# Performance work log

Hardware: AMD Instinct MI355X
Metric: run time of the kernel (lower is better)

## Reference

```python
import jax, jax.numpy as jnp
import numpy as np

EMBED = 384   # embeddingSize
BLOCK = 256   # blockSize (max T, also actual T here)
HEAD = 64     # headSize
B = 512
NEG_INF = -1e9  # stands in for float('-inf'); safe under fp16/bf16 via finite large value


def setup_inputs() -> dict:
    key = jax.random.key(0)
    k1, k2, k3, k4 = jax.random.split(key, 4)
    input = jax.random.normal(k1, (B, BLOCK, EMBED), dtype=jnp.float32)
    # nn.Linear(EMBED, HEAD, bias=False) weights, stored transposed for x @ W
    s = 1.0 / np.sqrt(EMBED)
    Wk = jax.random.uniform(k2, (EMBED, HEAD), dtype=jnp.float32, minval=-s, maxval=s)
    Wq = jax.random.uniform(k3, (EMBED, HEAD), dtype=jnp.float32, minval=-s, maxval=s)
    Wv = jax.random.uniform(k4, (EMBED, HEAD), dtype=jnp.float32, minval=-s, maxval=s)
    return {"input": input, "Wk": Wk, "Wq": Wq, "Wv": Wv}


def reference(input, Wk, Wq, Wv):
    B_, T, C = input.shape
    k = input @ Wk  # (B, T, H)
    q = input @ Wq  # (B, T, H)
    v = input @ Wv  # (B, T, H)
    # NOTE: original scales by C**-0.5 where C = embedding size (384), not head size.
    scale = jnp.asarray(C, input.dtype) ** -0.5
    weight = jnp.einsum('bth,bsh->bts', q, k) * scale  # (B, Tq, Tk)
    causal = jnp.tril(jnp.ones((T, T), dtype=bool))    # tril[:T,:T]
    weight = jnp.where(causal, weight, NEG_INF)
    # NOTE: original applies softmax over dim=1 (the QUERY axis), faithfully reproduced.
    weight = jax.nn.softmax(weight, axis=1)
    # dropout is identity in eval mode (deterministic reference)
    output = jnp.einsum('bts,bsh->bth', weight, v)     # (B, T, H)
    return output
```

## Files before the change

kernel.cpp:

```cpp
#include <hip/hip_runtime.h>
#include <hip/hip_bf16.h>

#define TT 256
#define CE 384
#define HD 64

typedef __attribute__((ext_vector_type(8))) short short8v;
typedef __attribute__((ext_vector_type(4))) float float4v;
typedef __attribute__((ext_vector_type(4))) unsigned int uint4v;
typedef __attribute__((ext_vector_type(4))) unsigned short ushort4v;

#define SCALE 0.05103103630798287f

__device__ __forceinline__ unsigned short f2bf(float f) {
    union { __hip_bfloat16 b; unsigned short u; } cv;
    cv.b = __float2bfloat16(f);
    return cv.u;
}
__device__ __forceinline__ unsigned int pk2(float a, float b) {
    return (unsigned int)f2bf(a) | ((unsigned int)f2bf(b) << 16);
}

__device__ __forceinline__ int adr8(int row, int col) {
    return row * 128 + ((((col >> 3) ^ (row & 7)) & 7) << 4) + ((col & 7) << 1);
}

#define BAR() do {                                            \
    asm volatile("s_waitcnt lgkmcnt(0)" ::: "memory");        \
    __builtin_amdgcn_s_barrier();                             \
    __builtin_amdgcn_sched_barrier(0);                        \
} while (0)

__global__ void wprep(const float* __restrict__ Wk, const float* __restrict__ Wq,
                      const float* __restrict__ Wv, unsigned short* __restrict__ Wt) {
    int idx = blockIdx.x * 256 + threadIdx.x;
    if (idx >= 3 * HD * CE) return;
    int w = idx / (HD * CE);
    int rem = idx - w * (HD * CE);
    int h = rem / CE;
    int c = rem - h * CE;
    const float* W = (w == 0) ? Wk : (w == 1) ? Wq : Wv;
    Wt[idx] = f2bf(W[c * HD + h]);
}

__global__ __launch_bounds__(512, 4)
void qkv(const float* __restrict__ X, const unsigned short* __restrict__ Wt,
         unsigned short* __restrict__ Kb, unsigned short* __restrict__ Qb,
         unsigned short* __restrict__ Vt) {
    __shared__ char lds[40960];
    char* Xs = lds;
    char* Ws = lds + 16384;

    const int bid = blockIdx.x;
    const int b = bid >> 1, rh = bid & 1;
    const int tid = threadIdx.x;
    const int w = tid >> 6, l = tid & 63;
    const int l15 = l & 15, lq = l >> 4;

    const float* Xb = X + ((long)b * TT + rh * 128) * CE;

    const int xt0 = tid >> 3,        xk0 = tid & 7;
    const int xt1 = 64 + (tid >> 3), xk1 = tid & 7;
    const int wn0 = tid >> 3;
    const int wn1 = 64 + (tid >> 3);
    const int wn2 = 128 + (tid >> 3);
    const int wk = tid & 7;

    float4 xa0, xa1, xb0, xb1;
    uint4v wr0, wr1, wr2;

    auto issue = [&](int kk) {
        const float* s0 = Xb + xt0 * CE + kk + xk0 * 8;
        xa0 = *(const float4*)s0;  xa1 = *(const float4*)(s0 + 4);
        const float* s1 = Xb + xt1 * CE + kk + xk1 * 8;
        xb0 = *(const float4*)s1;  xb1 = *(const float4*)(s1 + 4);
        wr0 = *(const uint4v*)(Wt + wn0 * CE + kk + wk * 8);
        wr1 = *(const uint4v*)(Wt + wn1 * CE + kk + wk * 8);
        wr2 = *(const uint4v*)(Wt + wn2 * CE + kk + wk * 8);
    };
    auto store = [&]() {
        uint4v p0 = {pk2(xa0.x, xa0.y), pk2(xa0.z, xa0.w), pk2(xa1.x, xa1.y), pk2(xa1.z, xa1.w)};
        *(uint4v*)(Xs + xt0 * 128 + (((xk0 ^ (xt0 & 7)) & 7) << 4)) = p0;
        uint4v p1 = {pk2(xb0.x, xb0.y), pk2(xb0.z, xb0.w), pk2(xb1.x, xb1.y), pk2(xb1.z, xb1.w)};
        *(uint4v*)(Xs + xt1 * 128 + (((xk1 ^ (xt1 & 7)) & 7) << 4)) = p1;
        *(uint4v*)(Ws + wn0 * 128 + (((wk ^ (wn0 & 7)) & 7) << 4)) = wr0;
        *(uint4v*)(Ws + wn1 * 128 + (((wk ^ (wn1 & 7)) & 7) << 4)) = wr1;
        *(uint4v*)(Ws + wn2 * 128 + (((wk ^ (wn2 & 7)) & 7) << 4)) = wr2;
    };

    const float4v fzero = {0.f, 0.f, 0.f, 0.f};
    float4v acc[12];
    #pragma unroll
    for (int j = 0; j < 12; ++j) acc[j] = fzero;

    issue(0);
    for (int kc = 0; kc < 6; ++kc) {
        BAR();
        store();
        if (kc < 5) issue((kc + 1) * 64);
        BAR();
        #pragma unroll
        for (int ks = 0; ks < 2; ++ks) {
            short8v a = *(const short8v*)(Xs + adr8(w * 16 + l15, ks * 32 + lq * 8));
            #pragma unroll
            for (int nt = 0; nt < 12; ++nt) {
                short8v bb = *(const short8v*)(Ws + adr8(nt * 16 + l15, ks * 32 + lq * 8));
                acc[nt] = __builtin_amdgcn_mfma_f32_16x16x32_bf16(a, bb, acc[nt], 0, 0, 0);
            }
        }
    }

    const int t0 = rh * 128 + w * 16 + lq * 4;
    #pragma unroll
    for (int nt = 0; nt < 12; ++nt) {
        const int n = nt * 16 + l15;
        if (n < 64) {
            #pragma unroll
            for (int r = 0; r < 4; ++r)
                Kb[((long)b * TT + t0 + r) * HD + n] = f2bf(acc[nt][r]);
        } else if (n < 128) {
            const int h = n - 64;
            #pragma unroll
            for (int r = 0; r < 4; ++r)
                Qb[((long)b * TT + t0 + r) * HD + h] = f2bf(acc[nt][r]);
        } else {
            const int h = n - 128;
            ushort4v pv;
            pv[0] = f2bf(acc[nt][0]);
            pv[1] = f2bf(acc[nt][1]);
            pv[2] = f2bf(acc[nt][2]);
            pv[3] = f2bf(acc[nt][3]);
            *(ushort4v*)(Vt + ((long)b * HD + h) * TT + t0) = pv;
        }
    }
}

__global__ __launch_bounds__(512, 4)
void attn(const unsigned short* __restrict__ Kb, const unsigned short* __restrict__ Qb,
          const unsigned short* __restrict__ Vt, float* __restrict__ out) {
    extern __shared__ char lds[];
    char* Qs  = lds;
    char* Wts = lds + 32768;
    char* Ks  = lds + 65536;
    char* Vts = lds + 73728;
    float2* smx = (float2*)Ks;

    const int b = blockIdx.x;
    const int tid = threadIdx.x;
    const int w = tid >> 6, l = tid & 63;
    const int l15 = l & 15, lq = l >> 4;
    const int sw = w & 3, th = w >> 2;

    #pragma unroll
    for (int j = 0; j < 4; ++j) {
        int ci = j * 512 + tid;
        int t = ci >> 3, k8 = ci & 7;
        uint4v p = *(const uint4v*)(Qb + ((long)b * TT + t) * HD + k8 * 8);
        *(uint4v*)(Qs + t * 128 + (((k8 ^ (t & 7)) & 7) << 4)) = p;
    }

    const float4v fzero = {0.f, 0.f, 0.f, 0.f};
    float4v o[2][4];
    #pragma unroll
    for (int i = 0; i < 2; ++i)
        #pragma unroll
        for (int j = 0; j < 4; ++j) o[i][j] = fzero;

    const int vrow = tid >> 3, vc8 = tid & 7;

    for (int sb = 0; sb < 4; ++sb) {
        const int s0 = sb * 64;
        __syncthreads();
        {
            uint4v pk = *(const uint4v*)(Kb + ((long)b * TT + s0 + vrow) * HD + vc8 * 8);
            *(uint4v*)(Ks + vrow * 128 + (((vc8 ^ (vrow & 7)) & 7) << 4)) = pk;
            uint4v pv = *(const uint4v*)(Vt + ((long)b * HD + vrow) * TT + s0 + vc8 * 8);
            *(uint4v*)(Vts + vrow * 128 + (((vc8 ^ (vrow & 7)) & 7) << 4)) = pv;
        }
        __syncthreads();

        float4v z[8];
        #pragma unroll
        for (int tt = 0; tt < 8; ++tt) z[tt] = fzero;
        #pragma unroll
        for (int ks = 0; ks < 2; ++ks) {
            short8v ak = *(const short8v*)(Ks + adr8(sw * 16 + l15, ks * 32 + lq * 8));
            #pragma unroll
            for (int tt = 0; tt < 8; ++tt) {
                short8v bq = *(const short8v*)(Qs + adr8(th * 128 + tt * 16 + l15, ks * 32 + lq * 8));
                z[tt] = __builtin_amdgcn_mfma_f32_16x16x32_bf16(ak, bq, z[tt], 0, 0, 0);
            }
        }
        __syncthreads();

        float pm[4], fac[4];
        #pragma unroll
        for (int r = 0; r < 4; ++r) {
            const int s = s0 + sw * 16 + lq * 4 + r;
            float mm = -1e30f;
            #pragma unroll
            for (int tt = 0; tt < 8; ++tt) {
                int t = th * 128 + tt * 16 + l15;
                float v = (t >= s) ? z[tt][r] * SCALE : -1e30f;
                z[tt][r] = v;
                mm = fmaxf(mm, v);
            }
            mm = fmaxf(mm, __shfl_xor(mm, 1));
            mm = fmaxf(mm, __shfl_xor(mm, 2));
            mm = fmaxf(mm, __shfl_xor(mm, 4));
            mm = fmaxf(mm, __shfl_xor(mm, 8));
            float ps = 0.f;
            #pragma unroll
            for (int tt = 0; tt < 8; ++tt) {
                float p = (z[tt][r] > -1e29f) ? __expf(z[tt][r] - mm) : 0.f;
                z[tt][r] = p;
                ps += p;
            }
            ps += __shfl_xor(ps, 1);
            ps += __shfl_xor(ps, 2);
            ps += __shfl_xor(ps, 4);
            ps += __shfl_xor(ps, 8);
            pm[r] = mm;
            if (l15 == 0) smx[th * 64 + sw * 16 + lq * 4 + r] = make_float2(mm, ps);
        }
        __syncthreads();

        #pragma unroll
        for (int r = 0; r < 4; ++r) {
            const int row = sw * 16 + lq * 4 + r;
            float2 h0 = smx[row];
            float2 h1 = smx[64 + row];
            float m = fmaxf(h0.x, h1.x);
            float denom = h0.y * __expf(h0.x - m) + h1.y * __expf(h1.x - m);
            fac[r] = __expf(pm[r] - m) / denom;
        }

        #pragma unroll
        for (int tt = 0; tt < 8; ++tt) {
            const int t = th * 128 + tt * 16 + l15;
            const int col = sw * 16 + lq * 4;
            ushort4v pw;
            pw[0] = f2bf(z[tt][0] * fac[0]);
            pw[1] = f2bf(z[tt][1] * fac[1]);
            pw[2] = f2bf(z[tt][2] * fac[2]);
            pw[3] = f2bf(z[tt][3] * fac[3]);
            *(ushort4v*)(Wts + t * 128 + ((((col >> 3) ^ (t & 7)) & 7) << 4) + ((col & 7) << 1)) = pw;
        }
        __syncthreads();

        #pragma unroll
        for (int ks = 0; ks < 2; ++ks) {
            short8v aw0 = *(const short8v*)(Wts + adr8(w * 32 + l15,      ks * 32 + lq * 8));
            short8v aw1 = *(const short8v*)(Wts + adr8(w * 32 + 16 + l15, ks * 32 + lq * 8));
            #pragma unroll
            for (int ht = 0; ht < 4; ++ht) {
                short8v bv = *(const short8v*)(Vts + adr8(ht * 16 + l15, ks * 32 + lq * 8));
                o[0][ht] = __builtin_amdgcn_mfma_f32_16x16x32_bf16(aw0, bv, o[0][ht], 0, 0, 0);
                o[1][ht] = __builtin_amdgcn_mfma_f32_16x16x32_bf16(aw1, bv, o[1][ht], 0, 0, 0);
            }
        }
    }

    #pragma unroll
    for (int rt = 0; rt < 2; ++rt)
        #pragma unroll
        for (int ht = 0; ht < 4; ++ht) {
            int t0 = w * 32 + rt * 16 + lq * 4;
            int h = ht * 16 + l15;
            #pragma unroll
            for (int r = 0; r < 4; ++r)
                out[((long)b * TT + t0 + r) * HD + h] = o[rt][ht][r];
        }
}

extern "C" void kernel_launch(void* const* d_in, const int* in_sizes, int n_in,
                              void* d_out, int out_size, void* d_ws, size_t ws_size,
                              hipStream_t stream) {
    const float* X  = (const float*)d_in[0];
    const float* Wk = (const float*)d_in[1];
    const float* Wq = (const float*)d_in[2];
    const float* Wv = (const float*)d_in[3];
    float* out = (float*)d_out;

    char* ws = (char*)d_ws;
    unsigned short* Wt = (unsigned short*)ws;
    unsigned short* Kb = (unsigned short*)(ws + 147456);
    unsigned short* Qb = (unsigned short*)(ws + 147456 + 16777216L);
    unsigned short* Vt = (unsigned short*)(ws + 147456 + 2 * 16777216L);

    (void)hipFuncSetAttribute(reinterpret_cast<const void*>(attn),
                              hipFuncAttributeMaxDynamicSharedMemorySize, 81920);

    wprep<<<288, 256, 0, stream>>>(Wk, Wq, Wv, Wt);
    qkv<<<1024, 512, 0, stream>>>(X, Wt, Kb, Qb, Vt);
    attn<<<512, 512, 81920, stream>>>(Kb, Qb, Vt, out);
}
```

Baseline: 85.55 us.

## Double-buffer LDS in qkv and prefetch K/V tiles in attn with priority hints

Result: slower. 109.0 us (+27.4%).

```diff
diff --git a/kernel.cpp b/kernel.cpp
--- a/kernel.cpp
+++ b/kernel.cpp
@@ -47,9 +47,7 @@
 void qkv(const float* __restrict__ X, const unsigned short* __restrict__ Wt,
          unsigned short* __restrict__ Kb, unsigned short* __restrict__ Qb,
          unsigned short* __restrict__ Vt) {
-    __shared__ char lds[40960];
-    char* Xs = lds;
-    char* Ws = lds + 16384;
+    extern __shared__ char lds[];
 
     const int bid = blockIdx.x;
     const int b = bid >> 1, rh = bid & 1;
@@ -66,23 +64,40 @@
     const int wn2 = 128 + (tid >> 3);
     const int wk = tid & 7;
 
-    float4 xa0, xa1, xb0, xb1;
+    float4 xa0, xa1, xa2, xa3;
+    float4 xb0, xb1, xb2, xb3;
     uint4v wr0, wr1, wr2;
 
-    auto issue = [&](int kk) {
+    auto issueXA = [&](int kk) {
         const float* s0 = Xb + xt0 * CE + kk + xk0 * 8;
         xa0 = *(const float4*)s0;  xa1 = *(const float4*)(s0 + 4);
         const float* s1 = Xb + xt1 * CE + kk + xk1 * 8;
-        xb0 = *(const float4*)s1;  xb1 = *(const float4*)(s1 + 4);
+        xa2 = *(const float4*)s1;  xa3 = *(const float4*)(s1 + 4);
+    };
+    auto issueXB = [&](int kk) {
+        const float* s0 = Xb + xt0 * CE + kk + xk0 * 8;
+        xb0 = *(const float4*)s0;  xb1 = *(const float4*)(s0 + 4);
+        const float* s1 = Xb + xt1 * CE + kk + xk1 * 8;
+        xb2 = *(const float4*)s1;  xb3 = *(const float4*)(s1 + 4);
+    };
+    auto issueW = [&](int kk) {
         wr0 = *(const uint4v*)(Wt + wn0 * CE + kk + wk * 8);
         wr1 = *(const uint4v*)(Wt + wn1 * CE + kk + wk * 8);
         wr2 = *(const uint4v*)(Wt + wn2 * CE + kk + wk * 8);
     };
-    auto store = [&]() {
+    auto storeXA = [&](char* Xs) {
         uint4v p0 = {pk2(xa0.x, xa0.y), pk2(xa0.z, xa0.w), pk2(xa1.x, xa1.y), pk2(xa1.z, xa1.w)};
         *(uint4v*)(Xs + xt0 * 128 + (((xk0 ^ (xt0 & 7)) & 7) << 4)) = p0;
-        uint4v p1 = {pk2(xb0.x, xb0.y), pk2(xb0.z, xb0.w), pk2(xb1.x, xb1.y), pk2(xb1.z, xb1.w)};
+        uint4v p1 = {pk2(xa2.x, xa2.y), pk2(xa2.z, xa2.w), pk2(xa3.x, xa3.y), pk2(xa3.z, xa3.w)};
         *(uint4v*)(Xs + xt1 * 128 + (((xk1 ^ (xt1 & 7)) & 7) << 4)) = p1;
+    };
+    auto storeXB = [&](char* Xs) {
+        uint4v p0 = {pk2(xb0.x, xb0.y), pk2(xb0.z, xb0.w), pk2(xb1.x, xb1.y), pk2(xb1.z, xb1.w)};
+        *(uint4v*)(Xs + xt0 * 128 + (((xk0 ^ (xt0 & 7)) & 7) << 4)) = p0;
+        uint4v p1 = {pk2(xb2.x, xb2.y), pk2(xb2.z, xb2.w), pk2(xb3.x, xb3.y), pk2(xb3.z, xb3.w)};
+        *(uint4v*)(Xs + xt1 * 128 + (((xk1 ^ (xt1 & 7)) & 7) << 4)) = p1;
+    };
+    auto storeW = [&](char* Ws) {
         *(uint4v*)(Ws + wn0 * 128 + (((wk ^ (wn0 & 7)) & 7) << 4)) = wr0;
         *(uint4v*)(Ws + wn1 * 128 + (((wk ^ (wn1 & 7)) & 7) << 4)) = wr1;
         *(uint4v*)(Ws + wn2 * 128 + (((wk ^ (wn2 & 7)) & 7) << 4)) = wr2;
@@ -93,12 +108,8 @@
     #pragma unroll
     for (int j = 0; j < 12; ++j) acc[j] = fzero;
 
-    issue(0);
-    for (int kc = 0; kc < 6; ++kc) {
-        BAR();
-        store();
-        if (kc < 5) issue((kc + 1) * 64);
-        BAR();
+    auto mfma_phase = [&](const char* Xs, const char* Ws) {
+        __builtin_amdgcn_s_setprio(1);
         #pragma unroll
         for (int ks = 0; ks < 2; ++ks) {
             short8v a = *(const short8v*)(Xs + adr8(w * 16 + l15, ks * 32 + lq * 8));
@@ -107,6 +118,32 @@
                 short8v bb = *(const short8v*)(Ws + adr8(nt * 16 + l15, ks * 32 + lq * 8));
                 acc[nt] = __builtin_amdgcn_mfma_f32_16x16x32_bf16(a, bb, acc[nt], 0, 0, 0);
             }
+        }
+        __builtin_amdgcn_s_setprio(0);
+    };
+
+    issueXA(0);
+    issueXB(64);
+    issueW(0);
+
+    #pragma unroll
+    for (int kp = 0; kp < 3; ++kp) {
+        {
+            char* Xs = lds;  char* Ws = lds + 16384;
+            storeXA(Xs);
+            storeW(Ws);
+            if (kp < 2) issueXA((2 * kp + 2) * 64);
+            issueW((2 * kp + 1) * 64);
+            BAR();
+            mfma_phase(Xs, Ws);
+        }
+        {
+            char* Xs = lds + 40960;  char* Ws = lds + 57344;
+            storeXB(Xs);
+            storeW(Ws);
+            if (kp < 2) { issueXB((2 * kp + 3) * 64); issueW((2 * kp + 2) * 64); }
+            BAR();
+            mfma_phase(Xs, Ws);
         }
     }
 
@@ -150,13 +187,23 @@
     const int w = tid >> 6, l = tid & 63;
     const int l15 = l & 15, lq = l >> 4;
     const int sw = w & 3, th = w >> 2;
+    const int vrow = tid >> 3, vc8 = tid & 7;
+
+    uint4v qreg[4];
+    #pragma unroll
+    for (int j = 0; j < 4; ++j) {
+        int ci = j * 512 + tid;
+        qreg[j] = *(const uint4v*)(Qb + ((long)b * TT + (ci >> 3)) * HD + (ci & 7) * 8);
+    }
+    uint4v pk[2], pv[2];
+    pk[0] = *(const uint4v*)(Kb + ((long)b * TT + vrow) * HD + vc8 * 8);
+    pv[0] = *(const uint4v*)(Vt + ((long)b * HD + vrow) * TT + vc8 * 8);
 
     #pragma unroll
     for (int j = 0; j < 4; ++j) {
         int ci = j * 512 + tid;
         int t = ci >> 3, k8 = ci & 7;
-        uint4v p = *(const uint4v*)(Qb + ((long)b * TT + t) * HD + k8 * 8);
-        *(uint4v*)(Qs + t * 128 + (((k8 ^ (t & 7)) & 7) << 4)) = p;
+        *(uint4v*)(Qs + t * 128 + (((k8 ^ (t & 7)) & 7) << 4)) = qreg[j];
     }
 
     const float4v fzero = {0.f, 0.f, 0.f, 0.f};
@@ -166,22 +213,24 @@
         #pragma unroll
         for (int j = 0; j < 4; ++j) o[i][j] = fzero;
 
-    const int vrow = tid >> 3, vc8 = tid & 7;
-
+    #pragma unroll
     for (int sb = 0; sb < 4; ++sb) {
         const int s0 = sb * 64;
-        __syncthreads();
-        {
-            uint4v pk = *(const uint4v*)(Kb + ((long)b * TT + s0 + vrow) * HD + vc8 * 8);
-            *(uint4v*)(Ks + vrow * 128 + (((vc8 ^ (vrow & 7)) & 7) << 4)) = pk;
-            uint4v pv = *(const uint4v*)(Vt + ((long)b * HD + vrow) * TT + s0 + vc8 * 8);
-            *(uint4v*)(Vts + vrow * 128 + (((vc8 ^ (vrow & 7)) & 7) << 4)) = pv;
-        }
-        __syncthreads();
+        const int cur = sb & 1;
+        BAR();
+
+        *(uint4v*)(Ks + vrow * 128 + (((vc8 ^ (vrow & 7)) & 7) << 4)) = pk[cur];
+        *(uint4v*)(Vts + vrow * 128 + (((vc8 ^ (vrow & 7)) & 7) << 4)) = pv[cur];
+        if (sb < 3) {
+            pk[cur ^ 1] = *(const uint4v*)(Kb + ((long)b * TT + s0 + 64 + vrow) * HD + vc8 * 8);
+            pv[cur ^ 1] = *(const uint4v*)(Vt + ((long)b * HD + vrow) * TT + s0 + 64 + vc8 * 8);
+        }
+        BAR();
 
         float4v z[8];
         #pragma unroll
         for (int tt = 0; tt < 8; ++tt) z[tt] = fzero;
+        __builtin_amdgcn_s_setprio(1);
         #pragma unroll
         for (int ks = 0; ks < 2; ++ks) {
             short8v ak = *(const short8v*)(Ks + adr8(sw * 16 + l15, ks * 32 + lq * 8));
@@ -191,7 +240,8 @@
                 z[tt] = __builtin_amdgcn_mfma_f32_16x16x32_bf16(ak, bq, z[tt], 0, 0, 0);
             }
         }
-        __syncthreads();
+        __builtin_amdgcn_s_setprio(0);
+        BAR();
 
         float pm[4], fac[4];
         #pragma unroll
@@ -223,7 +273,7 @@
             pm[r] = mm;
             if (l15 == 0) smx[th * 64 + sw * 16 + lq * 4 + r] = make_float2(mm, ps);
         }
-        __syncthreads();
+        BAR();
 
         #pragma unroll
         for (int r = 0; r < 4; ++r) {
@@ -246,8 +296,9 @@
             pw[3] = f2bf(z[tt][3] * fac[3]);
             *(ushort4v*)(Wts + t * 128 + ((((col >> 3) ^ (t & 7)) & 7) << 4) + ((col & 7) << 1)) = pw;
         }
-        __syncthreads();
-
+        BAR();
+
+        __builtin_amdgcn_s_setprio(1);
         #pragma unroll
         for (int ks = 0; ks < 2; ++ks) {
             short8v aw0 = *(const short8v*)(Wts + adr8(w * 32 + l15,      ks * 32 + lq * 8));
@@ -259,6 +310,7 @@
                 o[1][ht] = __builtin_amdgcn_mfma_f32_16x16x32_bf16(aw1, bv, o[1][ht], 0, 0, 0);
             }
         }
+        __builtin_amdgcn_s_setprio(0);
     }
 
     #pragma unroll
@@ -288,10 +340,12 @@
     unsigned short* Qb = (unsigned short*)(ws + 147456 + 16777216L);
     unsigned short* Vt = (unsigned short*)(ws + 147456 + 2 * 16777216L);
 
+    (void)hipFuncSetAttribute(reinterpret_cast<const void*>(qkv),
+                              hipFuncAttributeMaxDynamicSharedMemorySize, 81920);
     (void)hipFuncSetAttribute(reinterpret_cast<const void*>(attn),
                               hipFuncAttributeMaxDynamicSharedMemorySize, 81920);
 
     wprep<<<288, 256, 0, stream>>>(Wk, Wq, Wv, Wt);
-    qkv<<<1024, 512, 0, stream>>>(X, Wt, Kb, Qb, Vt);
+    qkv<<<1024, 512, 81920, stream>>>(X, Wt, Kb, Qb, Vt);
     attn<<<512, 512, 81920, stream>>>(Kb, Qb, Vt, out);
 }
```

## Load X and K fragments directly into registers and double-buffer prefetches

Applied to the files above, without the earlier changes.

Result: slower. 94.34 us (+10.3%).

```diff
diff --git a/kernel.cpp b/kernel.cpp
--- a/kernel.cpp
+++ b/kernel.cpp
@@ -20,6 +20,7 @@
 __device__ __forceinline__ unsigned int pk2(float a, float b) {
     return (unsigned int)f2bf(a) | ((unsigned int)f2bf(b) << 16);
 }
+union u4s8 { uint4v u; short8v s; };
 
 __device__ __forceinline__ int adr8(int row, int col) {
     return row * 128 + ((((col >> 3) ^ (row & 7)) & 7) << 4) + ((col & 7) << 1);
@@ -28,7 +29,6 @@
 #define BAR() do {                                            \
     asm volatile("s_waitcnt lgkmcnt(0)" ::: "memory");        \
     __builtin_amdgcn_s_barrier();                             \
-    __builtin_amdgcn_sched_barrier(0);                        \
 } while (0)
 
 __global__ void wprep(const float* __restrict__ Wk, const float* __restrict__ Wq,
@@ -47,9 +47,7 @@
 void qkv(const float* __restrict__ X, const unsigned short* __restrict__ Wt,
          unsigned short* __restrict__ Kb, unsigned short* __restrict__ Qb,
          unsigned short* __restrict__ Vt) {
-    __shared__ char lds[40960];
-    char* Xs = lds;
-    char* Ws = lds + 16384;
+    __shared__ char lds[49152];
 
     const int bid = blockIdx.x;
     const int b = bid >> 1, rh = bid & 1;
@@ -58,56 +56,65 @@
     const int l15 = l & 15, lq = l >> 4;
 
     const float* Xb = X + ((long)b * TT + rh * 128) * CE;
-
-    const int xt0 = tid >> 3,        xk0 = tid & 7;
-    const int xt1 = 64 + (tid >> 3), xk1 = tid & 7;
-    const int wn0 = tid >> 3;
-    const int wn1 = 64 + (tid >> 3);
-    const int wn2 = 128 + (tid >> 3);
+    const float* xrow = Xb + (w * 16 + l15) * CE + lq * 8;
+
+    const int wn0 = tid >> 3, wn1 = 64 + (tid >> 3), wn2 = 128 + (tid >> 3);
     const int wk = tid & 7;
 
-    float4 xa0, xa1, xb0, xb1;
     uint4v wr0, wr1, wr2;
-
-    auto issue = [&](int kk) {
-        const float* s0 = Xb + xt0 * CE + kk + xk0 * 8;
-        xa0 = *(const float4*)s0;  xa1 = *(const float4*)(s0 + 4);
-        const float* s1 = Xb + xt1 * CE + kk + xk1 * 8;
-        xb0 = *(const float4*)s1;  xb1 = *(const float4*)(s1 + 4);
+    auto issueW = [&](int kk) {
         wr0 = *(const uint4v*)(Wt + wn0 * CE + kk + wk * 8);
         wr1 = *(const uint4v*)(Wt + wn1 * CE + kk + wk * 8);
         wr2 = *(const uint4v*)(Wt + wn2 * CE + kk + wk * 8);
     };
-    auto store = [&]() {
-        uint4v p0 = {pk2(xa0.x, xa0.y), pk2(xa0.z, xa0.w), pk2(xa1.x, xa1.y), pk2(xa1.z, xa1.w)};
-        *(uint4v*)(Xs + xt0 * 128 + (((xk0 ^ (xt0 & 7)) & 7) << 4)) = p0;
-        uint4v p1 = {pk2(xb0.x, xb0.y), pk2(xb0.z, xb0.w), pk2(xb1.x, xb1.y), pk2(xb1.z, xb1.w)};
-        *(uint4v*)(Xs + xt1 * 128 + (((xk1 ^ (xt1 & 7)) & 7) << 4)) = p1;
+    auto storeW = [&](char* Ws) {
         *(uint4v*)(Ws + wn0 * 128 + (((wk ^ (wn0 & 7)) & 7) << 4)) = wr0;
         *(uint4v*)(Ws + wn1 * 128 + (((wk ^ (wn1 & 7)) & 7) << 4)) = wr1;
         *(uint4v*)(Ws + wn2 * 128 + (((wk ^ (wn2 & 7)) & 7) << 4)) = wr2;
     };
 
+    float4 xf[2][2][2];
+    auto issueX = [&](int set, int kk) {
+        #pragma unroll
+        for (int ks = 0; ks < 2; ++ks) {
+            xf[set][ks][0] = *(const float4*)(xrow + kk + ks * 32);
+            xf[set][ks][1] = *(const float4*)(xrow + kk + ks * 32 + 4);
+        }
+    };
+
     const float4v fzero = {0.f, 0.f, 0.f, 0.f};
     float4v acc[12];
     #pragma unroll
     for (int j = 0; j < 12; ++j) acc[j] = fzero;
 
-    issue(0);
-    for (int kc = 0; kc < 6; ++kc) {
-        BAR();
-        store();
-        if (kc < 5) issue((kc + 1) * 64);
-        BAR();
+    auto mfma_phase = [&](int set, const char* Ws) {
         #pragma unroll
         for (int ks = 0; ks < 2; ++ks) {
-            short8v a = *(const short8v*)(Xs + adr8(w * 16 + l15, ks * 32 + lq * 8));
+            u4s8 av;
+            av.u[0] = pk2(xf[set][ks][0].x, xf[set][ks][0].y);
+            av.u[1] = pk2(xf[set][ks][0].z, xf[set][ks][0].w);
+            av.u[2] = pk2(xf[set][ks][1].x, xf[set][ks][1].y);
+            av.u[3] = pk2(xf[set][ks][1].z, xf[set][ks][1].w);
             #pragma unroll
             for (int nt = 0; nt < 12; ++nt) {
                 short8v bb = *(const short8v*)(Ws + adr8(nt * 16 + l15, ks * 32 + lq * 8));
-                acc[nt] = __builtin_amdgcn_mfma_f32_16x16x32_bf16(a, bb, acc[nt], 0, 0, 0);
-            }
-        }
+                acc[nt] = __builtin_amdgcn_mfma_f32_16x16x32_bf16(av.s, bb, acc[nt], 0, 0, 0);
+            }
+        }
+    };
+
+    issueW(0);
+    issueX(0, 0);
+    issueX(1, 64);
+
+    #pragma unroll
+    for (int kc = 0; kc < 6; ++kc) {
+        char* Ws = lds + (kc & 1) * 24576;
+        storeW(Ws);
+        if (kc < 5) issueW((kc + 1) * 64);
+        BAR();
+        mfma_phase(kc & 1, Ws);
+        if (kc < 4) issueX(kc & 1, (kc + 2) * 64);
     }
 
     const int t0 = rh * 128 + w * 16 + lq * 4;
@@ -141,22 +148,34 @@
     extern __shared__ char lds[];
     char* Qs  = lds;
     char* Wts = lds + 32768;
-    char* Ks  = lds + 65536;
-    char* Vts = lds + 73728;
-    float2* smx = (float2*)Ks;
+    char* Vts = lds + 65536;
+    float2* smx = (float2*)(lds + 73728);
 
     const int b = blockIdx.x;
     const int tid = threadIdx.x;
     const int w = tid >> 6, l = tid & 63;
     const int l15 = l & 15, lq = l >> 4;
     const int sw = w & 3, th = w >> 2;
+    const int vrow = tid >> 3, vc8 = tid & 7;
+
+    const unsigned short* krow = Kb + ((long)b * TT + sw * 16 + l15) * HD + lq * 8;
+
+    uint4v qreg[4];
+    #pragma unroll
+    for (int j = 0; j < 4; ++j) {
+        int ci = j * 512 + tid;
+        qreg[j] = *(const uint4v*)(Qb + ((long)b * TT + (ci >> 3)) * HD + (ci & 7) * 8);
+    }
+    uint4v pv[2], kf[2][2];
+    pv[0] = *(const uint4v*)(Vt + ((long)b * HD + vrow) * TT + vc8 * 8);
+    kf[0][0] = *(const uint4v*)(krow);
+    kf[0][1] = *(const uint4v*)(krow + 32);
 
     #pragma unroll
     for (int j = 0; j < 4; ++j) {
         int ci = j * 512 + tid;
         int t = ci >> 3, k8 = ci & 7;
-        uint4v p = *(const uint4v*)(Qb + ((long)b * TT + t) * HD + k8 * 8);
-        *(uint4v*)(Qs + t * 128 + (((k8 ^ (t & 7)) & 7) << 4)) = p;
+        *(uint4v*)(Qs + t * 128 + (((k8 ^ (t & 7)) & 7) << 4)) = qreg[j];
     }
 
     const float4v fzero = {0.f, 0.f, 0.f, 0.f};
@@ -166,32 +185,31 @@
         #pragma unroll
         for (int j = 0; j < 4; ++j) o[i][j] = fzero;
 
-    const int vrow = tid >> 3, vc8 = tid & 7;
-
+    #pragma unroll
     for (int sb = 0; sb < 4; ++sb) {
         const int s0 = sb * 64;
-        __syncthreads();
-        {
-            uint4v pk = *(const uint4v*)(Kb + ((long)b * TT + s0 + vrow) * HD + vc8 * 8);
-            *(uint4v*)(Ks + vrow * 128 + (((vc8 ^ (vrow & 7)) & 7) << 4)) = pk;
-            uint4v pv = *(const uint4v*)(Vt + ((long)b * HD + vrow) * TT + s0 + vc8 * 8);
-            *(uint4v*)(Vts + vrow * 128 + (((vc8 ^ (vrow & 7)) & 7) << 4)) = pv;
-        }
-        __syncthreads();
+        const int cur = sb & 1, nxt = cur ^ 1;
+        BAR();
+
+        *(uint4v*)(Vts + vrow * 128 + (((vc8 ^ (vrow & 7)) & 7) << 4)) = pv[cur];
+        if (sb < 3) {
+            pv[nxt] = *(const uint4v*)(Vt + ((long)b * HD + vrow) * TT + s0 + 64 + vc8 * 8);
+            kf[nxt][0] = *(const uint4v*)(krow + (long)(s0 + 64) * HD);
+            kf[nxt][1] = *(const uint4v*)(krow + (long)(s0 + 64) * HD + 32);
+        }
 
         float4v z[8];
         #pragma unroll
         for (int tt = 0; tt < 8; ++tt) z[tt] = fzero;
         #pragma unroll
         for (int ks = 0; ks < 2; ++ks) {
-            short8v ak = *(const short8v*)(Ks + adr8(sw * 16 + l15, ks * 32 + lq * 8));
+            u4s8 ak; ak.u = kf[cur][ks];
             #pragma unroll
             for (int tt = 0; tt < 8; ++tt) {
                 short8v bq = *(const short8v*)(Qs + adr8(th * 128 + tt * 16 + l15, ks * 32 + lq * 8));
-                z[tt] = __builtin_amdgcn_mfma_f32_16x16x32_bf16(ak, bq, z[tt], 0, 0, 0);
-            }
-        }
-        __syncthreads();
+                z[tt] = __builtin_amdgcn_mfma_f32_16x16x32_bf16(ak.s, bq, z[tt], 0, 0, 0);
+            }
+        }
 
         float pm[4], fac[4];
         #pragma unroll
@@ -223,7 +241,7 @@
             pm[r] = mm;
             if (l15 == 0) smx[th * 64 + sw * 16 + lq * 4 + r] = make_float2(mm, ps);
         }
-        __syncthreads();
+        BAR();
 
         #pragma unroll
         for (int r = 0; r < 4; ++r) {
@@ -246,7 +264,7 @@
             pw[3] = f2bf(z[tt][3] * fac[3]);
             *(ushort4v*)(Wts + t * 128 + ((((col >> 3) ^ (t & 7)) & 7) << 4) + ((col & 7) << 1)) = pw;
         }
-        __syncthreads();
+        BAR();
 
         #pragma unroll
         for (int ks = 0; ks < 2; ++ks) {
@@ -289,9 +307,9 @@
     unsigned short* Vt = (unsigned short*)(ws + 147456 + 2 * 16777216L);
 
     (void)hipFuncSetAttribute(reinterpret_cast<const void*>(attn),
-                              hipFuncAttributeMaxDynamicSharedMemorySize, 81920);
+                              hipFuncAttributeMaxDynamicSharedMemorySize, 74752);
 
     wprep<<<288, 256, 0, stream>>>(Wk, Wq, Wv, Wt);
     qkv<<<1024, 512, 0, stream>>>(X, Wt, Kb, Qb, Vt);
-    attn<<<512, 512, 81920, stream>>>(Kb, Qb, Vt, out);
-}
+    attn<<<512, 512, 74752, stream>>>(Kb, Qb, Vt, out);
+}
```
